# Kernel tuning notes

Hardware: AMD Instinct MI355X
Metric: run time of the kernel (lower is better)

The kernel has to match this reference:

```python
import jax, jax.numpy as jnp
import numpy as np

B, S, D = 1024, 200, 128
NQ, NC, NQD, NCD = 50000, 1000, 101, 101


def _linear_params(k, fan_in, fan_out):
    bound = 1.0 / np.sqrt(fan_in)
    kw, kb = jax.random.split(k)
    W = jax.random.uniform(kw, (fan_out, fan_in), minval=-bound, maxval=bound, dtype=jnp.float32)
    b = jax.random.uniform(kb, (fan_out,), minval=-bound, maxval=bound, dtype=jnp.float32)
    return W, b


def setup_inputs() -> dict:
    key = jax.random.key(0)
    ks = jax.random.split(key, 17)
    Wx, bx = _linear_params(ks[0], 4 * D, D)
    Ws1, bs1 = _linear_params(ks[1], D, D)
    Ws2, bs2 = _linear_params(ks[2], D, D)
    Wp1, bp1 = _linear_params(ks[3], 2 * D, D)
    Wp2, bp2 = _linear_params(ks[4], 2 * D, D)
    Wk, bk = _linear_params(ks[5], 4 * D, D)
    Eq = jax.random.normal(ks[6], (NQ, D), dtype=jnp.float32)
    Ec = jax.random.normal(ks[7], (NC, D), dtype=jnp.float32)
    Eqd = jax.random.normal(ks[8], (NQD, D), dtype=jnp.float32)
    Ecd = jax.random.normal(ks[9], (NCD, D), dtype=jnp.float32)
    Ecorr = jax.random.normal(ks[10], (2, D), dtype=jnp.float32)
    # xavier_uniform init for h_pre (torch: gain*sqrt(6/(fan_in+fan_out)) on [B,D])
    bh = np.sqrt(6.0 / (B + D))
    h0 = jax.random.uniform(ks[11], (B, D), minval=-bh, maxval=bh, dtype=jnp.float32)
    question_seq = jax.random.randint(ks[12], (B, S), 0, NQ)
    concept_seq = jax.random.randint(ks[13], (B, S), 0, NC)
    question_diff_seq = jax.random.randint(ks[14], (B, S), 0, NQD)
    concept_diff_seq = jax.random.randint(ks[15], (B, S), 0, NCD)
    correct_seq = jax.random.randint(ks[16], (B, S), 0, 2)
    return dict(question_seq=question_seq, concept_seq=concept_seq,
                question_diff_seq=question_diff_seq, concept_diff_seq=concept_diff_seq,
                correct_seq=correct_seq,
                Eq=Eq, Ec=Ec, Eqd=Eqd, Ecd=Ecd, Ecorr=Ecorr,
                Wx=Wx, bx=bx, Ws1=Ws1, bs1=bs1, Ws2=Ws2, bs2=bs2,
                Wp1=Wp1, bp1=bp1, Wp2=Wp2, bp2=bp2, Wk=Wk, bk=bk, h0=h0)


def reference(question_seq, concept_seq, question_diff_seq, concept_diff_seq, correct_seq,
              Eq, Ec, Eqd, Ecd, Ecorr,
              Wx, bx, Ws1, bs1, Ws2, bs2, Wp1, bp1, Wp2, bp2, Wk, bk, h0):
    qe = Eq[question_seq]            # [B,S,D]
    ce = Ec[concept_seq]
    qde = Eqd[question_diff_seq]
    cde = Ecd[concept_diff_seq]
    corr = Ecorr[correct_seq]
    # generate_x_MLP applied to all timesteps at once (same math as per-step)
    x = jnp.concatenate([qe, ce, qde, cde], axis=-1) @ Wx.T + bx  # [B,S,D]
    # time-major inputs for the scan over t = 0 .. S-2
    xs = (jnp.swapaxes(x[:, :-1], 0, 1),      # x_t       [S-1,B,D]
          jnp.swapaxes(x[:, 1:], 0, 1),       # x_{t+1}
          jnp.swapaxes(corr[:, :-1], 0, 1),
          jnp.swapaxes(qde[:, :-1], 0, 1),
          jnp.swapaxes(cde[:, :-1], 0, 1))

    def step(h_pre, inp):
        xt, xnext, ct, qdt, cdt = inp
        s_in = xt - h_pre
        sdf = jax.nn.sigmoid(s_in @ Ws1.T + bs1) * jnp.tanh(s_in @ Ws2.T + bs2)  # dropout=eval identity
        p_in = jnp.concatenate([sdf, ct], axis=-1)
        pka = jax.nn.sigmoid(p_in @ Wp1.T + bp1) * jnp.tanh(p_in @ Wp2.T + bp2)
        k_in = jnp.concatenate([h_pre, ct, qdt, cdt], axis=-1)
        g = jax.nn.sigmoid(k_in @ Wk.T + bk)
        h = g * h_pre + (1.0 - g) * pka
        yt = jax.nn.sigmoid(jnp.sum(xnext * h, axis=-1))  # [B]
        return h, yt

    _, ys = jax.lax.scan(step, h0, xs)  # ys: [S-1,B]
    y = jnp.concatenate([ys.T, jnp.zeros((question_seq.shape[0], 1), x.dtype)], axis=1)  # [B,S], y[:, S-1]=0
    return y
```

## Files before the change

kernel.cpp:

```cpp
#include <hip/hip_runtime.h>
#include <hip/hip_bf16.h>


#define S_LEN 200
#define NBATCH 1024
#define DIM 128
#define LOG2E 1.4426950408889634f

typedef short short8 __attribute__((ext_vector_type(8)));
typedef float f32x4 __attribute__((ext_vector_type(4)));

__device__ __forceinline__ unsigned short f2b(float f) {
  union { float f; unsigned u; } v; v.f = f;
  unsigned r = (v.u + 0x7FFFu + ((v.u >> 16) & 1u)) >> 16;
  return (unsigned short)r;
}
__device__ __forceinline__ float b2f(unsigned short b) {
  union { unsigned u; float f; } v; v.u = ((unsigned)b) << 16;
  return v.f;
}
__device__ __forceinline__ unsigned pk_bf16(float lo, float hi) {
  __hip_bfloat162 t = __float22bfloat162_rn(make_float2(lo, hi));
  union { __hip_bfloat162 h; unsigned u; } cv; cv.h = t;
  return cv.u;
}
__device__ __forceinline__ float fast_sigmoid(float x) {
  return __builtin_amdgcn_rcpf(1.0f + __builtin_amdgcn_exp2f(-LOG2E * x));
}
__device__ __forceinline__ float fast_tanh(float x) {
  return 2.0f * __builtin_amdgcn_rcpf(1.0f + __builtin_amdgcn_exp2f(-2.0f * LOG2E * x)) - 1.0f;
}
__device__ __forceinline__ void wg_barrier_lds() {
  __asm__ volatile("s_waitcnt lgkmcnt(0)\n\ts_barrier" ::: "memory");
}

__global__ void proj_all_kernel(const float* __restrict__ Eq, const float* __restrict__ Ec,
                                const float* __restrict__ Eqd, const float* __restrict__ Ecd,
                                const float* __restrict__ Ecorr,
                                const float* __restrict__ Wx,
                                const float* __restrict__ Wp1, const float* __restrict__ bp1,
                                const float* __restrict__ Wp2, const float* __restrict__ bp2,
                                const float* __restrict__ Wk, const float* __restrict__ bk,
                                unsigned short* __restrict__ Tq, unsigned short* __restrict__ Tc,
                                unsigned short* __restrict__ Tqd, unsigned short* __restrict__ Tcd,
                                unsigned short* __restrict__ Tkqd, unsigned short* __restrict__ Tkcd,
                                float* __restrict__ Tkc, float* __restrict__ Tp1c,
                                float* __restrict__ Tp2c) {
  const int bid = blockIdx.x;
  const int tid = threadIdx.x;
  if (bid >= 802) {
    const int blk = bid - 802;
    if (blk < 101) {
      const int o = tid & 127, half = tid >> 7;
      const float* e = (half ? Ecd : Eqd) + (size_t)blk * DIM;
      const float* wr = Wk + (size_t)o * 512 + (half ? 384 : 256);
      float a = 0.f;
      for (int k = 0; k < DIM; ++k) a = fmaf(e[k], wr[k], a);
      (half ? Tkcd : Tkqd)[blk * DIM + o] = f2b(a);
    } else {
      for (int idx = tid; idx < 768; idx += 256) {
        const int t = idx >> 8, e = (idx >> 7) & 1, o = idx & 127;
        const float* ec = Ecorr + e * DIM;
        const float* wr; float bias; float* dst;
        if (t == 0)      { wr = Wp1 + (size_t)o * 256 + 128; bias = bp1[o]; dst = Tp1c; }
        else if (t == 1) { wr = Wp2 + (size_t)o * 256 + 128; bias = bp2[o]; dst = Tp2c; }
        else             { wr = Wk  + (size_t)o * 512 + 128; bias = bk[o];  dst = Tkc;  }
        float a = bias;
        for (int k = 0; k < DIM; ++k) a = fmaf(ec[k], wr[k], a);
        dst[e * DIM + o] = a;
      }
    }
    return;
  }
  const float* E; int M, coff, r0; unsigned short* T;
  if (bid < 782)      { E = Eq;  M = 50000; coff = 0;   T = Tq;  r0 = bid * 64; }
  else if (bid < 798) { E = Ec;  M = 1000;  coff = 128; T = Tc;  r0 = (bid - 782) * 64; }
  else if (bid < 800) { E = Eqd; M = 101;   coff = 256; T = Tqd; r0 = (bid - 798) * 64; }
  else                { E = Ecd; M = 101;   coff = 384; T = Tcd; r0 = (bid - 800) * 64; }

  __shared__ __align__(16) unsigned short A[64][136];
  {
    const int row = tid >> 2, cb = (tid & 3) * 32;
    union U8 { uint4 v; unsigned short s[8]; } o;
#pragma unroll
    for (int cc = 0; cc < 4; ++cc) {
      const int c8 = cb + cc * 8;
      if (r0 + row < M) {
        const float4 e0 = *(const float4*)(E + (size_t)(r0 + row) * DIM + c8);
        const float4 e1 = *(const float4*)(E + (size_t)(r0 + row) * DIM + c8 + 4);
        o.s[0] = f2b(e0.x); o.s[1] = f2b(e0.y); o.s[2] = f2b(e0.z); o.s[3] = f2b(e0.w);
        o.s[4] = f2b(e1.x); o.s[5] = f2b(e1.y); o.s[6] = f2b(e1.z); o.s[7] = f2b(e1.w);
      } else {
        o.v = make_uint4(0, 0, 0, 0);
      }
      *(uint4*)&A[row][c8] = o.v;
    }
  }
  __syncthreads();
  const int w = tid >> 6, L = tid & 63, q = L >> 4, m = L & 15;
  short8 bf[2][4];
#pragma unroll
  for (int T2 = 0; T2 < 2; ++T2) {
    const int n = 32 * w + 16 * T2 + m;
#pragma unroll
    for (int kb = 0; kb < 4; ++kb) {
      const float* src = Wx + (size_t)n * 512 + coff + kb * 32 + q * 8;
      const float4 v0 = *(const float4*)src;
      const float4 v1 = *(const float4*)(src + 4);
      short8 f;
      f[0] = (short)f2b(v0.x); f[1] = (short)f2b(v0.y);
      f[2] = (short)f2b(v0.z); f[3] = (short)f2b(v0.w);
      f[4] = (short)f2b(v1.x); f[5] = (short)f2b(v1.y);
      f[6] = (short)f2b(v1.z); f[7] = (short)f2b(v1.w);
      bf[T2][kb] = f;
    }
  }
  const f32x4 vzero = {0.f, 0.f, 0.f, 0.f};
#pragma unroll
  for (int mt = 0; mt < 4; ++mt) {
    short8 af[4];
#pragma unroll
    for (int kb = 0; kb < 4; ++kb) af[kb] = *(const short8*)&A[mt * 16 + m][kb * 32 + q * 8];
    f32x4 acc[2] = {vzero, vzero};
#pragma unroll
    for (int kb = 0; kb < 4; ++kb) {
#pragma unroll
      for (int T2 = 0; T2 < 2; ++T2)
        acc[T2] = __builtin_amdgcn_mfma_f32_16x16x32_bf16(af[kb], bf[T2][kb], acc[T2], 0, 0, 0);
    }
#pragma unroll
    for (int T2 = 0; T2 < 2; ++T2) {
      const int col = 32 * w + 16 * T2 + m;
#pragma unroll
      for (int i = 0; i < 4; ++i) {
        const int r = r0 + mt * 16 + q * 4 + i;
        if (r < M) T[(size_t)r * DIM + col] = f2b(acc[T2][i]);
      }
    }
  }
}

__global__ void build_x_kernel(const int* __restrict__ qs, const int* __restrict__ cs,
                               const int* __restrict__ qds, const int* __restrict__ cds,
                               const int* __restrict__ corr,
                               const unsigned short* __restrict__ Tq, const unsigned short* __restrict__ Tc,
                               const unsigned short* __restrict__ Tqd, const unsigned short* __restrict__ Tcd,
                               const float* __restrict__ bx, unsigned short* __restrict__ xg,
                               float* __restrict__ SSg, float* __restrict__ corrf) {
  const int r = blockIdx.x * 16 + (threadIdx.x >> 4);
  const int c8 = (threadIdx.x & 15) * 8;
  const int s = r >> 10, b = r & 1023;
  const int q = qs[b * S_LEN + s], c = cs[b * S_LEN + s];
  const int qd = qds[b * S_LEN + s], cd = cds[b * S_LEN + s];
  union U8 { uint4 v; unsigned short s[8]; };
  U8 vq, vc, vd, ve, o;
  vq.v = *(const uint4*)(Tq + (size_t)q * DIM + c8);
  vc.v = *(const uint4*)(Tc + (size_t)c * DIM + c8);
  vd.v = *(const uint4*)(Tqd + (size_t)qd * DIM + c8);
  ve.v = *(const uint4*)(Tcd + (size_t)cd * DIM + c8);
  const float4 bx0 = *(const float4*)(bx + c8);
  const float4 bx1 = *(const float4*)(bx + c8 + 4);
  float bb[8] = {bx0.x, bx0.y, bx0.z, bx0.w, bx1.x, bx1.y, bx1.z, bx1.w};
  float part = 0.f;
#pragma unroll
  for (int j = 0; j < 8; ++j) {
    const float sv = b2f(vq.s[j]) + b2f(vc.s[j]) + b2f(vd.s[j]) + b2f(ve.s[j]) + bb[j];
    o.s[j] = f2b(sv);
    const float xr = b2f(o.s[j]);
    part = fmaf(xr, xr, part);
  }
  *(uint4*)(xg + (size_t)r * DIM + c8) = o.v;
#pragma unroll
  for (int off = 1; off <= 8; off <<= 1) part += __shfl_xor(part, off, 64);
  if ((threadIdx.x & 15) == 0) {
    SSg[r] = part;
    corrf[r] = (float)corr[b * S_LEN + s];
  }
}

__global__ void gemm_xg_kernel(const unsigned short* __restrict__ xg,
                               const float* __restrict__ Wk,
                               const int* __restrict__ corr, const int* __restrict__ qds,
                               const int* __restrict__ cds,
                               const float* __restrict__ Tkc,
                               const unsigned short* __restrict__ Tkqd,
                               const unsigned short* __restrict__ Tkcd,
                               unsigned short* __restrict__ GG) {
  const int tid = threadIdx.x;
  const int r0 = blockIdx.x * 64;
  __shared__ __align__(16) unsigned short TS[64][136];
  {
    const int row = tid >> 2, cb = (tid & 3) * 32;
    const int r = r0 + row, t = r >> 10, b = r & 1023;
    const int ci = corr[b * S_LEN + t], qi = qds[b * S_LEN + t], di = cds[b * S_LEN + t];
    union U8 { uint4 v; unsigned short s[8]; };
#pragma unroll
    for (int cc = 0; cc < 4; ++cc) {
      const int c8 = cb + cc * 8;
      U8 vq, vc, o;
      vq.v = *(const uint4*)(Tkqd + (size_t)qi * DIM + c8);
      vc.v = *(const uint4*)(Tkcd + (size_t)di * DIM + c8);
      const float4 k0 = *(const float4*)(Tkc + (size_t)ci * DIM + c8);
      const float4 k1 = *(const float4*)(Tkc + (size_t)ci * DIM + c8 + 4);
      float kk[8] = {k0.x, k0.y, k0.z, k0.w, k1.x, k1.y, k1.z, k1.w};
#pragma unroll
      for (int j = 0; j < 8; ++j) o.s[j] = f2b(kk[j] + b2f(vq.s[j]) + b2f(vc.s[j]));
      *(uint4*)&TS[row][c8] = o.v;
    }
  }
  __syncthreads();
  const int w = tid >> 6, L = tid & 63, q = L >> 4, m = L & 15;
  short8 wk[2][4];
#pragma unroll
  for (int T = 0; T < 2; ++T) {
    const int n = 32 * w + 16 * T + m;
#pragma unroll
    for (int kb = 0; kb < 4; ++kb) {
      const float* src = Wk + (size_t)n * 512 + kb * 32 + q * 8;
      const float4 v0 = *(const float4*)src;
      const float4 v1 = *(const float4*)(src + 4);
      short8 f;
      f[0] = (short)f2b(v0.x); f[1] = (short)f2b(v0.y);
      f[2] = (short)f2b(v0.z); f[3] = (short)f2b(v0.w);
      f[4] = (short)f2b(v1.x); f[5] = (short)f2b(v1.y);
      f[6] = (short)f2b(v1.z); f[7] = (short)f2b(v1.w);
      wk[T][kb] = f;
    }
  }
  const f32x4 vzero = {0.f, 0.f, 0.f, 0.f};
#pragma unroll
  for (int mt = 0; mt < 4; ++mt) {
    short8 af[4];
#pragma unroll
    for (int kb = 0; kb < 4; ++kb)
      af[kb] = *(const short8*)(xg + (size_t)(r0 + mt * 16 + m) * DIM + kb * 32 + q * 8);
    f32x4 acc[2] = {vzero, vzero};
#pragma unroll
    for (int kb = 0; kb < 4; ++kb) {
#pragma unroll
      for (int T = 0; T < 2; ++T)
        acc[T] = __builtin_amdgcn_mfma_f32_16x16x32_bf16(af[kb], wk[T][kb], acc[T], 0, 0, 0);
    }
#pragma unroll
    for (int T = 0; T < 2; ++T) {
      const int col = 32 * w + 16 * T + m;
#pragma unroll
      for (int i = 0; i < 4; ++i) {
        const int row64 = mt * 16 + q * 4 + i;
        GG[(size_t)(r0 + row64) * DIM + col] = f2b(acc[T][i] + b2f(TS[row64][col]));
      }
    }
  }
}

__global__ __launch_bounds__(512, 2) void scan_kernel(
    const unsigned short* __restrict__ xg,
    const unsigned short* __restrict__ gg,
    const float* __restrict__ SSg,
    const float* __restrict__ corrf,
    const float* __restrict__ h0,
    const float* __restrict__ Ws1, const float* __restrict__ bs1,
    const float* __restrict__ Ws2, const float* __restrict__ bs2,
    const float* __restrict__ Wp1, const float* __restrict__ Wp2,
    const float* __restrict__ Wk,
    const float* __restrict__ gTp1c, const float* __restrict__ gTp2c,
    float* __restrict__ outp) {
  __shared__ __align__(16) unsigned short Sbuf[16][136];
  __shared__ __align__(16) unsigned short Pbuf[16][136];

  const int tid = threadIdx.x;
  const int w = tid >> 6, L = tid & 63, q = L >> 4, m = L & 15;
  const int col16 = 16 * w + m;
  const int rbase = blockIdx.x << 4;
  const size_t SB = (size_t)NBATCH * DIM;

  short8 wf[5][4];
  {
    const float* Wptr[5] = {Ws1, Ws2, Wp1, Wp2, Wk};
    const int ldw[5] = {128, 128, 256, 256, 512};
#pragma unroll
    for (int M = 0; M < 5; ++M) {
#pragma unroll
      for (int kb = 0; kb < 4; ++kb) {
        const float* src = Wptr[M] + (size_t)col16 * ldw[M] + kb * 32 + q * 8;
        const float4 v0 = *(const float4*)src;
        const float4 v1 = *(const float4*)(src + 4);
        short8 f;
        f[0] = (short)f2b(v0.x); f[1] = (short)f2b(v0.y);
        f[2] = (short)f2b(v0.z); f[3] = (short)f2b(v0.w);
        f[4] = (short)f2b(v1.x); f[5] = (short)f2b(v1.y);
        f[6] = (short)f2b(v1.z); f[7] = (short)f2b(v1.w);
        wf[M][kb] = f;
      }
    }
  }
  const float bs1v = bs1[col16], bs2v = bs2[col16];
  const float tp1v0 = gTp1c[col16], dtp1 = gTp1c[DIM + col16] - tp1v0;
  const float tp2v0 = gTp2c[col16], dtp2 = gTp2c[DIM + col16] - tp2v0;

  float h[4];
#pragma unroll
  for (int i = 0; i < 4; ++i) {
    const int b = rbase + q * 4 + i;
    const float hv = h0[(size_t)b * DIM + col16];
    h[i] = hv;
    const float xt = b2f(xg[(size_t)b * DIM + col16]);
    Sbuf[q * 4 + i][col16] = f2b(xt - hv);
  }
  if (tid < 16) outp[(size_t)(rbase + tid) * S_LEN + (S_LEN - 1)] = 0.0f;
  float* poy = outp + (size_t)(rbase + m) * S_LEN;

  unsigned short XPA[4], XPB[4], GPA[4], GPB[4];
  float4 CFA, CFB;
  short8 XFA[4], XFB[4];
  float SSA, SSB;
  const unsigned short* pxA = xg + 3 * SB + (size_t)(rbase + q * 4) * DIM + col16;
  const unsigned short* pxB = pxA + SB;
  const unsigned short* pgA = gg + 2 * SB + (size_t)(rbase + q * 4) * DIM + col16;
  const unsigned short* pgB = pgA + SB;
  const float* pcA = corrf + 2 * NBATCH + rbase + q * 4;
  const float* pcB = pcA + NBATCH;
  const unsigned short* pfA = xg + 2 * SB + (size_t)(rbase + m) * DIM + q * 8;
  const unsigned short* pfB = pfA + SB;
  const float* psA = SSg + 2 * NBATCH + rbase + m;
  const float* psB = psA + NBATCH;
#pragma unroll
  for (int i = 0; i < 4; ++i) {
    XPA[i] = xg[SB + (size_t)(rbase + q * 4 + i) * DIM + col16];
    XPB[i] = xg[2 * SB + (size_t)(rbase + q * 4 + i) * DIM + col16];
    GPA[i] = gg[(size_t)(rbase + q * 4 + i) * DIM + col16];
    GPB[i] = gg[SB + (size_t)(rbase + q * 4 + i) * DIM + col16];
  }
  CFA = *(const float4*)(corrf + rbase + q * 4);
  CFB = *(const float4*)(corrf + NBATCH + rbase + q * 4);
#pragma unroll
  for (int kb = 0; kb < 4; ++kb) {
    XFA[kb] = *(const short8*)(xg + (size_t)(rbase + m) * DIM + kb * 32 + q * 8);
    XFB[kb] = *(const short8*)(xg + SB + (size_t)(rbase + m) * DIM + kb * 32 + q * 8);
  }
  SSA = SSg[rbase + m];
  SSB = SSg[NBATCH + rbase + m];

  const f32x4 vzero = {0.f, 0.f, 0.f, 0.f};

#define STEP(TCUR, XP, GP, CF, PX, PG, PC, XF, SSR, PF, PS)                    \
  do {                                                                         \
    const int t_ = (TCUR);                                                     \
    float xnv[4], ggv[4], cfv[4];                                              \
    _Pragma("unroll") for (int i = 0; i < 4; ++i) {                            \
      xnv[i] = b2f(XP[i]); ggv[i] = b2f(GP[i]);                                \
    }                                                                          \
    cfv[0] = CF.x; cfv[1] = CF.y; cfv[2] = CF.z; cfv[3] = CF.w;                \
    short8 xfr[4]; float ssv = SSR;                                            \
    if (w == 0) {                                                              \
      _Pragma("unroll") for (int kb = 0; kb < 4; ++kb) xfr[kb] = XF[kb];       \
    }                                                                          \
    _Pragma("unroll") for (int i = 0; i < 4; ++i) {                            \
      XP[i] = PX[i * DIM]; GP[i] = PG[i * DIM];                                \
    }                                                                          \
    CF = *(const float4*)PC;                                                   \
    PX += 2 * SB; PG += 2 * SB; PC += 2 * NBATCH;                              \
    if (w == 0) {                                                              \
      _Pragma("unroll") for (int kb = 0; kb < 4; ++kb)                         \
        XF[kb] = *(const short8*)(PF + kb * 32);                               \
      SSR = *PS;                                                               \
      PF += 2 * SB; PS += 2 * NBATCH;                                          \
    }                                                                          \
    wg_barrier_lds();                                       \
    short8 sf[4];                                                              \
    _Pragma("unroll") for (int kb = 0; kb < 4; ++kb)                           \
        sf[kb] = *(const short8*)&Sbuf[m][kb * 32 + q * 8];                    \
    f32x4 a1 = vzero, a2 = vzero, c1 = vzero;                                  \
    _Pragma("unroll") for (int kb = 0; kb < 4; ++kb) {                         \
      a1 = __builtin_amdgcn_mfma_f32_16x16x32_bf16(sf[kb], wf[0][kb], a1, 0, 0, 0); \
      a2 = __builtin_amdgcn_mfma_f32_16x16x32_bf16(sf[kb], wf[1][kb], a2, 0, 0, 0); \
      c1 = __builtin_amdgcn_mfma_f32_16x16x32_bf16(sf[kb], wf[4][kb], c1, 0, 0, 0); \
    }                                                                          \
    if (w == 0) {                                                              \
      f32x4 dt = vzero;                                                        \
      _Pragma("unroll") for (int kb = 0; kb < 4; ++kb)                         \
        dt = __builtin_amdgcn_mfma_f32_16x16x32_bf16(sf[kb], xfr[kb], dt, 0, 0, 0); \
      if (t_ > 0 && q == (m >> 2)) {                                           \
        const int ii = m & 3;                                                  \
        const float D = ii == 0 ? dt[0] : ii == 1 ? dt[1] : ii == 2 ? dt[2] : dt[3]; \
        poy[t_ - 1] = fast_sigmoid(ssv - D);                                   \
      }                                                                        \
    }                                                                          \
    _Pragma("unroll") for (int i2 = 0; i2 < 2; ++i2) {                         \
      const float s0 = fast_sigmoid(a1[2 * i2] + bs1v) * fast_tanh(a2[2 * i2] + bs2v); \
      const float s1 = fast_sigmoid(a1[2 * i2 + 1] + bs1v) * fast_tanh(a2[2 * i2 + 1] + bs2v); \
      const unsigned u = pk_bf16(s0, s1);                                      \
      Pbuf[q * 4 + 2 * i2][col16] = (unsigned short)u;                         \
      Pbuf[q * 4 + 2 * i2 + 1][col16] = (unsigned short)(u >> 16);             \
    }                                                                          \
    wg_barrier_lds();                                          \
    short8 pf[4];                                                              \
    _Pragma("unroll") for (int kb = 0; kb < 4; ++kb)                           \
        pf[kb] = *(const short8*)&Pbuf[m][kb * 32 + q * 8];                    \
    f32x4 p1 = vzero, p2 = vzero;                                              \
    _Pragma("unroll") for (int kb = 0; kb < 4; ++kb) {                         \
      p1 = __builtin_amdgcn_mfma_f32_16x16x32_bf16(pf[kb], wf[2][kb], p1, 0, 0, 0); \
      p2 = __builtin_amdgcn_mfma_f32_16x16x32_bf16(pf[kb], wf[3][kb], p2, 0, 0, 0); \
    }                                                                          \
    float sn[4];                                                               \
    _Pragma("unroll") for (int i = 0; i < 4; ++i) {                            \
      const float g = fast_sigmoid(ggv[i] - c1[i]);                            \
      const float t1v = fmaf(cfv[i], dtp1, tp1v0);                             \
      const float t2v = fmaf(cfv[i], dtp2, tp2v0);                             \
      const float pka = fast_sigmoid(p1[i] + t1v) * fast_tanh(p2[i] + t2v);    \
      const float hn = pka + g * (h[i] - pka);                                 \
      h[i] = hn;                                                               \
      sn[i] = xnv[i] - hn;                                                     \
    }                                                                          \
    _Pragma("unroll") for (int i2 = 0; i2 < 2; ++i2) {                         \
      const unsigned u = pk_bf16(sn[2 * i2], sn[2 * i2 + 1]);                  \
      Sbuf[q * 4 + 2 * i2][col16] = (unsigned short)u;                         \
      Sbuf[q * 4 + 2 * i2 + 1][col16] = (unsigned short)(u >> 16);             \
    }                                                                          \
  } while (0)

  for (int t2 = 0; t2 < 198; t2 += 2) {
    STEP(t2, XPA, GPA, CFA, pxA, pgA, pcA, XFA, SSA, pfA, psA);
    STEP(t2 + 1, XPB, GPB, CFB, pxB, pgB, pcB, XFB, SSB, pfB, psB);
  }
  STEP(198, XPA, GPA, CFA, pxA, pgA, pcA, XFA, SSA, pfA, psA);
#undef STEP

  wg_barrier_lds();
  if (w == 0) {
    short8 sf[4];
#pragma unroll
    for (int kb = 0; kb < 4; ++kb) sf[kb] = *(const short8*)&Sbuf[m][kb * 32 + q * 8];
    f32x4 dt = vzero;
#pragma unroll
    for (int kb = 0; kb < 4; ++kb)
      dt = __builtin_amdgcn_mfma_f32_16x16x32_bf16(sf[kb], XFB[kb], dt, 0, 0, 0);
    if (q == (m >> 2)) {
      const int ii = m & 3;
      const float D = ii == 0 ? dt[0] : ii == 1 ? dt[1] : ii == 2 ? dt[2] : dt[3];
      poy[S_LEN - 2] = fast_sigmoid(SSB - D);
    }
  }
}

extern "C" void kernel_launch(void* const* d_in, const int* in_sizes, int n_in,
                              void* d_out, int out_size, void* d_ws, size_t ws_size,
                              hipStream_t stream) {
  const int* qs    = (const int*)d_in[0];
  const int* cs    = (const int*)d_in[1];
  const int* qds   = (const int*)d_in[2];
  const int* cds   = (const int*)d_in[3];
  const int* corr  = (const int*)d_in[4];
  const float* Eq    = (const float*)d_in[5];
  const float* Ec    = (const float*)d_in[6];
  const float* Eqd   = (const float*)d_in[7];
  const float* Ecd   = (const float*)d_in[8];
  const float* Ecorr = (const float*)d_in[9];
  const float* Wx  = (const float*)d_in[10];
  const float* bx  = (const float*)d_in[11];
  const float* Ws1 = (const float*)d_in[12];
  const float* bs1 = (const float*)d_in[13];
  const float* Ws2 = (const float*)d_in[14];
  const float* bs2 = (const float*)d_in[15];
  const float* Wp1 = (const float*)d_in[16];
  const float* bp1 = (const float*)d_in[17];
  const float* Wp2 = (const float*)d_in[18];
  const float* bp2 = (const float*)d_in[19];
  const float* Wk  = (const float*)d_in[20];
  const float* bk  = (const float*)d_in[21];
  const float* h0  = (const float*)d_in[22];

  char* ws = (char*)d_ws;
  const size_t xbytes = (size_t)S_LEN * NBATCH * DIM * 2;
  const size_t A = (xbytes + 255) & ~(size_t)255;
  const size_t ggbytes = (size_t)(S_LEN - 1) * NBATCH * DIM * 2;
  unsigned short* X  = (unsigned short*)ws;
  unsigned short* GG = (unsigned short*)(ws + A);
  unsigned short* Tq  = GG;
  unsigned short* Tc  = (unsigned short*)(ws + A + (size_t)50000 * DIM * 2);
  unsigned short* Tqd = (unsigned short*)(ws + A + (size_t)51000 * DIM * 2);
  unsigned short* Tcd = (unsigned short*)(ws + A + (size_t)51101 * DIM * 2);
  size_t off = A + ((ggbytes + 255) & ~(size_t)255);
  auto alloc = [&](size_t bytes) {
    void* p = ws + off;
    off = (off + bytes + 255) & ~(size_t)255;
    return p;
  };
  float* corrf = (float*)alloc((size_t)S_LEN * NBATCH * 4);
  float* SS    = (float*)alloc((size_t)S_LEN * NBATCH * 4);
  unsigned short* Tkqd = (unsigned short*)alloc((size_t)101 * DIM * 2);
  unsigned short* Tkcd = (unsigned short*)alloc((size_t)101 * DIM * 2);
  float* Tkc  = (float*)alloc((size_t)2 * DIM * 4);
  float* Tp1c = (float*)alloc((size_t)2 * DIM * 4);
  float* Tp2c = (float*)alloc((size_t)2 * DIM * 4);

  proj_all_kernel<<<904, 256, 0, stream>>>(Eq, Ec, Eqd, Ecd, Ecorr, Wx,
                                           Wp1, bp1, Wp2, bp2, Wk, bk,
                                           Tq, Tc, Tqd, Tcd, Tkqd, Tkcd, Tkc, Tp1c, Tp2c);
  build_x_kernel<<<(S_LEN * NBATCH) / 16, 256, 0, stream>>>(qs, cs, qds, cds, corr,
                                                            Tq, Tc, Tqd, Tcd, bx, X, SS, corrf);
  gemm_xg_kernel<<<((S_LEN - 1) * NBATCH) / 64, 256, 0, stream>>>(X, Wk, corr, qds, cds,
                                                                  Tkc, Tkqd, Tkcd, GG);
  scan_kernel<<<64, 512, 0, stream>>>(X, GG, SS, corrf, h0, Ws1, bs1, Ws2, bs2,
                                      Wp1, Wp2, Wk, Tp1c, Tp2c, (float*)d_out);
}
```

Before: 513.7 us.

## Compute output dot from registers, fuse sigmoid-tanh, enlarge gather and GEMM tiles

```diff
diff --git a/kernel.cpp b/kernel.cpp
--- a/kernel.cpp
+++ b/kernel.cpp
@@ -24,11 +24,16 @@
   union { __hip_bfloat162 h; unsigned u; } cv; cv.h = t;
   return cv.u;
 }
+__device__ __forceinline__ float sigtanh(float a, float b) {
+  a = fminf(a, 30.0f);
+  b = fminf(b, 15.0f);
+  const float u = __builtin_amdgcn_exp2f(LOG2E * a);
+  const float v = __builtin_amdgcn_exp2f(2.0f * LOG2E * b);
+  return (u * (v - 1.0f)) * __builtin_amdgcn_rcpf((1.0f + u) * (v + 1.0f));
+}
 __device__ __forceinline__ float fast_sigmoid(float x) {
+  x = fmaxf(x, -30.0f);
   return __builtin_amdgcn_rcpf(1.0f + __builtin_amdgcn_exp2f(-LOG2E * x));
-}
-__device__ __forceinline__ float fast_tanh(float x) {
-  return 2.0f * __builtin_amdgcn_rcpf(1.0f + __builtin_amdgcn_exp2f(-2.0f * LOG2E * x)) - 1.0f;
 }
 __device__ __forceinline__ void wg_barrier_lds() {
   __asm__ volatile("s_waitcnt lgkmcnt(0)\n\ts_barrier" ::: "memory");
@@ -146,35 +151,29 @@
                                const unsigned short* __restrict__ Tq, const unsigned short* __restrict__ Tc,
                                const unsigned short* __restrict__ Tqd, const unsigned short* __restrict__ Tcd,
                                const float* __restrict__ bx, unsigned short* __restrict__ xg,
-                               float* __restrict__ SSg, float* __restrict__ corrf) {
-  const int r = blockIdx.x * 16 + (threadIdx.x >> 4);
+                               float* __restrict__ corrf) {
+  const int r0 = blockIdx.x * 32;
   const int c8 = (threadIdx.x & 15) * 8;
-  const int s = r >> 10, b = r & 1023;
-  const int q = qs[b * S_LEN + s], c = cs[b * S_LEN + s];
-  const int qd = qds[b * S_LEN + s], cd = cds[b * S_LEN + s];
-  union U8 { uint4 v; unsigned short s[8]; };
-  U8 vq, vc, vd, ve, o;
-  vq.v = *(const uint4*)(Tq + (size_t)q * DIM + c8);
-  vc.v = *(const uint4*)(Tc + (size_t)c * DIM + c8);
-  vd.v = *(const uint4*)(Tqd + (size_t)qd * DIM + c8);
-  ve.v = *(const uint4*)(Tcd + (size_t)cd * DIM + c8);
   const float4 bx0 = *(const float4*)(bx + c8);
   const float4 bx1 = *(const float4*)(bx + c8 + 4);
   float bb[8] = {bx0.x, bx0.y, bx0.z, bx0.w, bx1.x, bx1.y, bx1.z, bx1.w};
-  float part = 0.f;
-#pragma unroll
-  for (int j = 0; j < 8; ++j) {
-    const float sv = b2f(vq.s[j]) + b2f(vc.s[j]) + b2f(vd.s[j]) + b2f(ve.s[j]) + bb[j];
-    o.s[j] = f2b(sv);
-    const float xr = b2f(o.s[j]);
-    part = fmaf(xr, xr, part);
-  }
-  *(uint4*)(xg + (size_t)r * DIM + c8) = o.v;
-#pragma unroll
-  for (int off = 1; off <= 8; off <<= 1) part += __shfl_xor(part, off, 64);
-  if ((threadIdx.x & 15) == 0) {
-    SSg[r] = part;
-    corrf[r] = (float)corr[b * S_LEN + s];
+  union U8 { uint4 v; unsigned short s[8]; };
+#pragma unroll
+  for (int half = 0; half < 2; ++half) {
+    const int r = r0 + (threadIdx.x >> 4) + half * 16;
+    const int s = r >> 10, b = r & 1023;
+    const int q = qs[b * S_LEN + s], c = cs[b * S_LEN + s];
+    const int qd = qds[b * S_LEN + s], cd = cds[b * S_LEN + s];
+    U8 vq, vc, vd, ve, o;
+    vq.v = *(const uint4*)(Tq + (size_t)q * DIM + c8);
+    vc.v = *(const uint4*)(Tc + (size_t)c * DIM + c8);
+    vd.v = *(const uint4*)(Tqd + (size_t)qd * DIM + c8);
+    ve.v = *(const uint4*)(Tcd + (size_t)cd * DIM + c8);
+#pragma unroll
+    for (int j = 0; j < 8; ++j)
+      o.s[j] = f2b(b2f(vq.s[j]) + b2f(vc.s[j]) + b2f(vd.s[j]) + b2f(ve.s[j]) + bb[j]);
+    *(uint4*)(xg + (size_t)r * DIM + c8) = o.v;
+    if ((threadIdx.x & 15) == 0) corrf[r] = (float)corr[b * S_LEN + s];
   }
 }
 
@@ -187,10 +186,12 @@
                                const unsigned short* __restrict__ Tkcd,
                                unsigned short* __restrict__ GG) {
   const int tid = threadIdx.x;
-  const int r0 = blockIdx.x * 64;
-  __shared__ __align__(16) unsigned short TS[64][136];
-  {
-    const int row = tid >> 2, cb = (tid & 3) * 32;
+  const int r0 = blockIdx.x * 128;
+  __shared__ __align__(16) unsigned short TS[128][136];
+#pragma unroll
+  for (int it = 0; it < 2; ++it) {
+    const int idx = tid + 256 * it;
+    const int row = idx >> 2, cb = (idx & 3) * 32;
     const int r = r0 + row, t = r >> 10, b = r & 1023;
     const int ci = corr[b * S_LEN + t], qi = qds[b * S_LEN + t], di = cds[b * S_LEN + t];
     union U8 { uint4 v; unsigned short s[8]; };
@@ -229,7 +230,7 @@
   }
   const f32x4 vzero = {0.f, 0.f, 0.f, 0.f};
 #pragma unroll
-  for (int mt = 0; mt < 4; ++mt) {
+  for (int mt = 0; mt < 8; ++mt) {
     short8 af[4];
 #pragma unroll
     for (int kb = 0; kb < 4; ++kb)
@@ -246,8 +247,8 @@
       const int col = 32 * w + 16 * T + m;
 #pragma unroll
       for (int i = 0; i < 4; ++i) {
-        const int row64 = mt * 16 + q * 4 + i;
-        GG[(size_t)(r0 + row64) * DIM + col] = f2b(acc[T][i] + b2f(TS[row64][col]));
+        const int row128 = mt * 16 + q * 4 + i;
+        GG[(size_t)(r0 + row128) * DIM + col] = f2b(acc[T][i] + b2f(TS[row128][col]));
       }
     }
   }
@@ -256,7 +257,6 @@
 __global__ __launch_bounds__(512, 2) void scan_kernel(
     const unsigned short* __restrict__ xg,
     const unsigned short* __restrict__ gg,
-    const float* __restrict__ SSg,
     const float* __restrict__ corrf,
     const float* __restrict__ h0,
     const float* __restrict__ Ws1, const float* __restrict__ bs1,
@@ -267,6 +267,7 @@
     float* __restrict__ outp) {
   __shared__ __align__(16) unsigned short Sbuf[16][136];
   __shared__ __align__(16) unsigned short Pbuf[16][136];
+  __shared__ float DotBuf[16][9];
 
   const int tid = threadIdx.x;
   const int w = tid >> 6, L = tid & 63, q = L >> 4, m = L & 15;
@@ -308,22 +309,15 @@
     Sbuf[q * 4 + i][col16] = f2b(xt - hv);
   }
   if (tid < 16) outp[(size_t)(rbase + tid) * S_LEN + (S_LEN - 1)] = 0.0f;
-  float* poy = outp + (size_t)(rbase + m) * S_LEN;
 
   unsigned short XPA[4], XPB[4], GPA[4], GPB[4];
   float4 CFA, CFB;
-  short8 XFA[4], XFB[4];
-  float SSA, SSB;
   const unsigned short* pxA = xg + 3 * SB + (size_t)(rbase + q * 4) * DIM + col16;
   const unsigned short* pxB = pxA + SB;
   const unsigned short* pgA = gg + 2 * SB + (size_t)(rbase + q * 4) * DIM + col16;
   const unsigned short* pgB = pgA + SB;
   const float* pcA = corrf + 2 * NBATCH + rbase + q * 4;
   const float* pcB = pcA + NBATCH;
-  const unsigned short* pfA = xg + 2 * SB + (size_t)(rbase + m) * DIM + q * 8;
-  const unsigned short* pfB = pfA + SB;
-  const float* psA = SSg + 2 * NBATCH + rbase + m;
-  const float* psB = psA + NBATCH;
 #pragma unroll
   for (int i = 0; i < 4; ++i) {
     XPA[i] = xg[SB + (size_t)(rbase + q * 4 + i) * DIM + col16];
@@ -333,70 +327,65 @@
   }
   CFA = *(const float4*)(corrf + rbase + q * 4);
   CFB = *(const float4*)(corrf + NBATCH + rbase + q * 4);
-#pragma unroll
-  for (int kb = 0; kb < 4; ++kb) {
-    XFA[kb] = *(const short8*)(xg + (size_t)(rbase + m) * DIM + kb * 32 + q * 8);
-    XFB[kb] = *(const short8*)(xg + SB + (size_t)(rbase + m) * DIM + kb * 32 + q * 8);
-  }
-  SSA = SSg[rbase + m];
-  SSB = SSg[NBATCH + rbase + m];
-
+
+  float dotp[4] = {0.f, 0.f, 0.f, 0.f};
   const f32x4 vzero = {0.f, 0.f, 0.f, 0.f};
 
-#define STEP(TCUR, XP, GP, CF, PX, PG, PC, XF, SSR, PF, PS)                    \
+#define STEP(TCUR, XP, GP, CF, PX, PG, PC)                                     \
   do {                                                                         \
     const int t_ = (TCUR);                                                     \
+    wg_barrier_lds();                  \
+      \
+    short8 sf[4];                                                              \
+    _Pragma("unroll") for (int kb = 0; kb < 4; ++kb)                           \
+        sf[kb] = *(const short8*)&Sbuf[m][kb * 32 + q * 8];                    \
     float xnv[4], ggv[4], cfv[4];                                              \
     _Pragma("unroll") for (int i = 0; i < 4; ++i) {                            \
       xnv[i] = b2f(XP[i]); ggv[i] = b2f(GP[i]);                                \
     }                                                                          \
     cfv[0] = CF.x; cfv[1] = CF.y; cfv[2] = CF.z; cfv[3] = CF.w;                \
-    short8 xfr[4]; float ssv = SSR;                                            \
-    if (w == 0) {                                                              \
-      _Pragma("unroll") for (int kb = 0; kb < 4; ++kb) xfr[kb] = XF[kb];       \
-    }                                                                          \
     _Pragma("unroll") for (int i = 0; i < 4; ++i) {                            \
       XP[i] = PX[i * DIM]; GP[i] = PG[i * DIM];                                \
     }                                                                          \
     CF = *(const float4*)PC;                                                   \
     PX += 2 * SB; PG += 2 * SB; PC += 2 * NBATCH;                              \
-    if (w == 0) {                                                              \
-      _Pragma("unroll") for (int kb = 0; kb < 4; ++kb)                         \
-        XF[kb] = *(const short8*)(PF + kb * 32);                               \
-      SSR = *PS;                                                               \
-      PF += 2 * SB; PS += 2 * NBATCH;                                          \
-    }                                                                          \
-    wg_barrier_lds();                                       \
-    short8 sf[4];                                                              \
-    _Pragma("unroll") for (int kb = 0; kb < 4; ++kb)                           \
-        sf[kb] = *(const short8*)&Sbuf[m][kb * 32 + q * 8];                    \
+    {                  \
+      float dr0 = dotp[0], dr1 = dotp[1], dr2 = dotp[2], dr3 = dotp[3];        \
+      _Pragma("unroll") for (int off = 1; off <= 8; off <<= 1) {               \
+        dr0 += __shfl_xor(dr0, off, 64);                                       \
+        dr1 += __shfl_xor(dr1, off, 64);                                       \
+        dr2 += __shfl_xor(dr2, off, 64);                                       \
+        dr3 += __shfl_xor(dr3, off, 64);                                       \
+      }                                                                        \
+      if (m == 0) {                                                            \
+        DotBuf[q * 4 + 0][w] = dr0;                                            \
+        DotBuf[q * 4 + 1][w] = dr1;                                            \
+        DotBuf[q * 4 + 2][w] = dr2;                                            \
+        DotBuf[q * 4 + 3][w] = dr3;                                            \
+      }                                                                        \
+    }                                                                          \
     f32x4 a1 = vzero, a2 = vzero, c1 = vzero;                                  \
     _Pragma("unroll") for (int kb = 0; kb < 4; ++kb) {                         \
       a1 = __builtin_amdgcn_mfma_f32_16x16x32_bf16(sf[kb], wf[0][kb], a1, 0, 0, 0); \
       a2 = __builtin_amdgcn_mfma_f32_16x16x32_bf16(sf[kb], wf[1][kb], a2, 0, 0, 0); \
       c1 = __builtin_amdgcn_mfma_f32_16x16x32_bf16(sf[kb], wf[4][kb], c1, 0, 0, 0); \
     }                                                                          \
-    if (w == 0) {                                                              \
-      f32x4 dt = vzero;                                                        \
-      _Pragma("unroll") for (int kb = 0; kb < 4; ++kb)                         \
-        dt = __builtin_amdgcn_mfma_f32_16x16x32_bf16(sf[kb], xfr[kb], dt, 0, 0, 0); \
-      if (t_ > 0 && q == (m >> 2)) {                                           \
-        const int ii = m & 3;                                                  \
-        const float D = ii == 0 ? dt[0] : ii == 1 ? dt[1] : ii == 2 ? dt[2] : dt[3]; \
-        poy[t_ - 1] = fast_sigmoid(ssv - D);                                   \
-      }                                                                        \
-    }                                                                          \
     _Pragma("unroll") for (int i2 = 0; i2 < 2; ++i2) {                         \
-      const float s0 = fast_sigmoid(a1[2 * i2] + bs1v) * fast_tanh(a2[2 * i2] + bs2v); \
-      const float s1 = fast_sigmoid(a1[2 * i2 + 1] + bs1v) * fast_tanh(a2[2 * i2 + 1] + bs2v); \
+      const float s0 = sigtanh(a1[2 * i2] + bs1v, a2[2 * i2] + bs2v);          \
+      const float s1 = sigtanh(a1[2 * i2 + 1] + bs1v, a2[2 * i2 + 1] + bs2v);  \
       const unsigned u = pk_bf16(s0, s1);                                      \
       Pbuf[q * 4 + 2 * i2][col16] = (unsigned short)u;                         \
       Pbuf[q * 4 + 2 * i2 + 1][col16] = (unsigned short)(u >> 16);             \
     }                                                                          \
-    wg_barrier_lds();                                          \
+    wg_barrier_lds();                                 \
     short8 pf[4];                                                              \
     _Pragma("unroll") for (int kb = 0; kb < 4; ++kb)                           \
         pf[kb] = *(const short8*)&Pbuf[m][kb * 32 + q * 8];                    \
+    if (t_ > 0 && tid < 16) {          \
+      float d = 0.f;                                                           \
+      _Pragma("unroll") for (int ww = 0; ww < 8; ++ww) d += DotBuf[tid][ww];   \
+      outp[(size_t)(rbase + tid) * S_LEN + (t_ - 1)] = fast_sigmoid(d);        \
+    }                                                                          \
     f32x4 p1 = vzero, p2 = vzero;                                              \
     _Pragma("unroll") for (int kb = 0; kb < 4; ++kb) {                         \
       p1 = __builtin_amdgcn_mfma_f32_16x16x32_bf16(pf[kb], wf[2][kb], p1, 0, 0, 0); \
@@ -407,10 +396,11 @@
       const float g = fast_sigmoid(ggv[i] - c1[i]);                            \
       const float t1v = fmaf(cfv[i], dtp1, tp1v0);                             \
       const float t2v = fmaf(cfv[i], dtp2, tp2v0);                             \
-      const float pka = fast_sigmoid(p1[i] + t1v) * fast_tanh(p2[i] + t2v);    \
+      const float pka = sigtanh(p1[i] + t1v, p2[i] + t2v);                     \
       const float hn = pka + g * (h[i] - pka);                                 \
       h[i] = hn;                                                               \
       sn[i] = xnv[i] - hn;                                                     \
+      dotp[i] = xnv[i] * hn;                                                   \
     }                                                                          \
     _Pragma("unroll") for (int i2 = 0; i2 < 2; ++i2) {                         \
       const unsigned u = pk_bf16(sn[2 * i2], sn[2 * i2 + 1]);                  \
@@ -420,26 +410,34 @@
   } while (0)
 
   for (int t2 = 0; t2 < 198; t2 += 2) {
-    STEP(t2, XPA, GPA, CFA, pxA, pgA, pcA, XFA, SSA, pfA, psA);
-    STEP(t2 + 1, XPB, GPB, CFB, pxB, pgB, pcB, XFB, SSB, pfB, psB);
-  }
-  STEP(198, XPA, GPA, CFA, pxA, pgA, pcA, XFA, SSA, pfA, psA);
+    STEP(t2, XPA, GPA, CFA, pxA, pgA, pcA);
+    STEP(t2 + 1, XPB, GPB, CFB, pxB, pgB, pcB);
+  }
+  STEP(198, XPA, GPA, CFA, pxA, pgA, pcA);
 #undef STEP
 
+  {
+    float dr0 = dotp[0], dr1 = dotp[1], dr2 = dotp[2], dr3 = dotp[3];
+#pragma unroll
+    for (int off = 1; off <= 8; off <<= 1) {
+      dr0 += __shfl_xor(dr0, off, 64);
+      dr1 += __shfl_xor(dr1, off, 64);
+      dr2 += __shfl_xor(dr2, off, 64);
+      dr3 += __shfl_xor(dr3, off, 64);
+    }
+    if (m == 0) {
+      DotBuf[q * 4 + 0][w] = dr0;
+      DotBuf[q * 4 + 1][w] = dr1;
+      DotBuf[q * 4 + 2][w] = dr2;
+      DotBuf[q * 4 + 3][w] = dr3;
+    }
+  }
   wg_barrier_lds();
-  if (w == 0) {
-    short8 sf[4];
-#pragma unroll
-    for (int kb = 0; kb < 4; ++kb) sf[kb] = *(const short8*)&Sbuf[m][kb * 32 + q * 8];
-    f32x4 dt = vzero;
-#pragma unroll
-    for (int kb = 0; kb < 4; ++kb)
-      dt = __builtin_amdgcn_mfma_f32_16x16x32_bf16(sf[kb], XFB[kb], dt, 0, 0, 0);
-    if (q == (m >> 2)) {
-      const int ii = m & 3;
-      const float D = ii == 0 ? dt[0] : ii == 1 ? dt[1] : ii == 2 ? dt[2] : dt[3];
-      poy[S_LEN - 2] = fast_sigmoid(SSB - D);
-    }
+  if (tid < 16) {
+    float d = 0.f;
+#pragma unroll
+    for (int ww = 0; ww < 8; ++ww) d += DotBuf[tid][ww];
+    outp[(size_t)(rbase + tid) * S_LEN + (S_LEN - 2)] = fast_sigmoid(d);
   }
 }
 
@@ -487,7 +485,6 @@
     return p;
   };
   float* corrf = (float*)alloc((size_t)S_LEN * NBATCH * 4);
-  float* SS    = (float*)alloc((size_t)S_LEN * NBATCH * 4);
   unsigned short* Tkqd = (unsigned short*)alloc((size_t)101 * DIM * 2);
   unsigned short* Tkcd = (unsigned short*)alloc((size_t)101 * DIM * 2);
   float* Tkc  = (float*)alloc((size_t)2 * DIM * 4);
@@ -497,10 +494,10 @@
   proj_all_kernel<<<904, 256, 0, stream>>>(Eq, Ec, Eqd, Ecd, Ecorr, Wx,
                                            Wp1, bp1, Wp2, bp2, Wk, bk,
                                            Tq, Tc, Tqd, Tcd, Tkqd, Tkcd, Tkc, Tp1c, Tp2c);
-  build_x_kernel<<<(S_LEN * NBATCH) / 16, 256, 0, stream>>>(qs, cs, qds, cds, corr,
-                                                            Tq, Tc, Tqd, Tcd, bx, X, SS, corrf);
-  gemm_xg_kernel<<<((S_LEN - 1) * NBATCH) / 64, 256, 0, stream>>>(X, Wk, corr, qds, cds,
-                                                                  Tkc, Tkqd, Tkcd, GG);
-  scan_kernel<<<64, 512, 0, stream>>>(X, GG, SS, corrf, h0, Ws1, bs1, Ws2, bs2,
+  build_x_kernel<<<(S_LEN * NBATCH) / 32, 256, 0, stream>>>(qs, cs, qds, cds, corr,
+                                                            Tq, Tc, Tqd, Tcd, bx, X, corrf);
+  gemm_xg_kernel<<<((S_LEN - 1) * NBATCH) / 128, 256, 0, stream>>>(X, Wk, corr, qds, cds,
+                                                                   Tkc, Tkqd, Tkcd, GG);
+  scan_kernel<<<64, 512, 0, stream>>>(X, GG, corrf, h0, Ws1, bs1, Ws2, bs2,
                                       Wp1, Wp2, Wk, Tp1c, Tp2c, (float*)d_out);
 }
```

Measured after the change: 546.9 us. +6.5%, slower.
